# Performance work log

Hardware: AMD Instinct MI355X
Metric: run time of the kernel (lower is better)

Reference implementation:

```python
import jax, jax.numpy as jnp
import numpy as np

EPS = 1e-5
S_CENTERS = 1024  # npoint//4
NSAMPLE = 32


def index_points(pts, idx):
    # pts [B,N,C], idx [B,...] int -> [B,...,C]
    return jax.vmap(lambda p, i: p[i])(pts, idx)


def farthest_point_sample(xyz, npoint):
    # xyz [B,N,3] -> [B,npoint] indices (deterministic start at index 0)
    B, N, _ = xyz.shape
    def body(carry, _):
        dist, far = carry
        centroid = jnp.take_along_axis(xyz, far[:, None, None], axis=1)  # [B,1,3]
        d = jnp.sum((xyz - centroid) ** 2, axis=-1)                      # [B,N]
        dist = jnp.minimum(dist, d)
        nxt = jnp.argmax(dist, axis=-1).astype(jnp.int32)
        return (dist, nxt), far
    init = (jnp.full((B, N), 1e10, xyz.dtype), jnp.zeros((B,), jnp.int32))
    _, idx = jax.lax.scan(body, init, None, length=npoint)
    return jnp.transpose(idx)  # [B,npoint]


def knn_point(k, xyz, new_xyz):
    # squared dists [B,S,N], take k nearest
    d = (jnp.sum(new_xyz ** 2, -1)[:, :, None]
         + jnp.sum(xyz ** 2, -1)[:, None, :]
         - 2.0 * jnp.einsum('bsc,bnc->bsn', new_xyz, xyz))
    _, idx = jax.lax.top_k(-d, k)
    return idx  # [B,S,k]


def instance_norm(h):
    # h [B,S,K,C]: InstanceNorm2d (affine=False) normalizes per (b,c) over spatial dims
    mu = jnp.mean(h, axis=(1, 2), keepdims=True)
    var = jnp.var(h, axis=(1, 2), keepdims=True)
    return (h - mu) * jax.lax.rsqrt(var + EPS)


def setup_inputs() -> dict:
    key = jax.random.key(0)
    ks = jax.random.split(key, 12)
    B, N, C = 8, 4096, 128
    inp = {
        'pc1_l_loc2': jax.random.normal(ks[0], (B, 3, N), jnp.float32),
        'corr_feats': jax.random.normal(ks[1], (B, C, N), jnp.float32),
        'W1': jax.random.normal(ks[2], (128, 131), jnp.float32) * 0.05,
        'b1': jnp.zeros((128,), jnp.float32),
        'W2': jax.random.normal(ks[3], (128, 128), jnp.float32) * 0.05,
        'b2': jnp.zeros((128,), jnp.float32),
        'W3': jax.random.normal(ks[4], (128, 128), jnp.float32) * 0.05,
        'b3': jnp.zeros((128,), jnp.float32),
        'fc_w': jax.random.normal(ks[5], (3, 128), jnp.float32) * 0.05,
        'fc_b': jnp.zeros((3,), jnp.float32),
    }
    return inp


def reference(pc1_l_loc2, corr_feats, W1, b1, W2, b2, W3, b3, fc_w, fc_b):
    xyz = jnp.transpose(pc1_l_loc2, (0, 2, 1))    # [B,N,3]
    points = jnp.transpose(corr_feats, (0, 2, 1))  # [B,N,128]

    fps_idx = farthest_point_sample(xyz, S_CENTERS)           # [B,S]
    new_xyz = index_points(xyz, fps_idx)                      # [B,S,3]
    idx = knn_point(NSAMPLE, xyz, new_xyz)                    # [B,S,K]
    grouped_xyz = index_points(xyz, idx)                      # [B,S,K,3]
    grouped_xyz_norm = grouped_xyz - new_xyz[:, :, None, :]
    grouped_pts = index_points(points, idx)                   # [B,S,K,128]
    h = jnp.concatenate([grouped_xyz_norm, grouped_pts], -1)  # [B,S,K,131]

    for W, b in ((W1, b1), (W2, b2), (W3, b3)):
        h = jnp.einsum('bskc,oc->bsko', h, W) + b  # 1x1 conv as matmul
        h = jax.nn.relu(instance_norm(h))

    x = jnp.max(h, axis=2)                         # [B,S,128] max over neighbors
    x = jnp.einsum('bsc,oc->bso', x, fc_w) + fc_b  # [B,S,3]
    flow0 = jnp.transpose(x, (0, 2, 1))            # [B,3,S]
    return flow0
```

## Files before the change

### kernel.cpp

```cpp
#include <hip/hip_runtime.h>
#include <hip/hip_fp16.h>

#define NB 8
#define NPTS 4096
#define NS 1024
#define NK 32
#define NM (NB*NS*NK)

typedef _Float16 f16x8 __attribute__((ext_vector_type(8)));
typedef float    f32x4 __attribute__((ext_vector_type(4)));
typedef float    f32x2 __attribute__((ext_vector_type(2)));

__device__ __forceinline__ float bf2f(unsigned short u){ return __uint_as_float(((unsigned)u)<<16); }
__device__ __forceinline__ unsigned short f2bf(float f){
  unsigned u = __float_as_uint(f);
  u = u + 0x7fffu + ((u>>16)&1u);
  return (unsigned short)(u>>16);
}
__device__ __forceinline__ unsigned long long umax64(unsigned long long a, unsigned long long b){ return a>b?a:b; }

#define DPP_STEP_MAX(x, ctrl, rm) { \
  unsigned _t = (unsigned)__builtin_amdgcn_update_dpp((int)(x), (int)(x), (ctrl), (rm), 0xf, false); \
  (x) = ((x) > _t) ? (x) : _t; }

__device__ __forceinline__ unsigned wave_max_u32(unsigned x){
  DPP_STEP_MAX(x, 0x111, 0xf);
  DPP_STEP_MAX(x, 0x112, 0xf);
  DPP_STEP_MAX(x, 0x114, 0xf);
  DPP_STEP_MAX(x, 0x118, 0xf);
  DPP_STEP_MAX(x, 0x142, 0xa);
  DPP_STEP_MAX(x, 0x143, 0xc);
  return (unsigned)__builtin_amdgcn_readlane((int)x, 63);
}

__device__ __forceinline__ bool detect_f32(const unsigned short* __restrict__ u){
  int huge_=0, zero_=0;
  #pragma unroll
  for (int i=0;i<64;i++){
    unsigned short w = u[i];
    if ((w & 0x7fffu) == 0) { zero_++; continue; }
    float a = fabsf(bf2f(w));
    if (a > 1e6f || a < 1e-6f) huge_++;
  }
  return (huge_ >= 8) || (zero_ >= 24);
}
__device__ __forceinline__ float ldin(const void* p, size_t i, bool f32){
  if (f32) return ((const float*)p)[i];
  else     return bf2f(((const unsigned short*)p)[i]);
}

__global__ __launch_bounds__(256) void fps_kernel(const void* __restrict__ pc1,
                                                  int* __restrict__ fps_out){
  __shared__ __align__(16) float4 cp4[NPTS];
  __shared__ __align__(16) unsigned long long part[2][4];
  int b = blockIdx.x, t = threadIdx.x;
  const bool f32 = detect_f32((const unsigned short*)pc1);
  const size_t base = (size_t)b*3*NPTS;
  for (int i=t;i<NPTS;i+=256){
    float4 v;
    v.x = ldin(pc1, base+i, f32);
    v.y = ldin(pc1, base+NPTS+i, f32);
    v.z = ldin(pc1, base+2*NPTS+i, f32);
    v.w = 0.f;
    cp4[i] = v;
  }
  __syncthreads();
  f32x2 px[8],py[8],pz[8],dist[8];
  #pragma unroll
  for (int j=0;j<8;j++){
    float4 a = cp4[t*16+2*j], c = cp4[t*16+2*j+1];
    px[j] = f32x2{a.x, c.x};
    py[j] = f32x2{a.y, c.y};
    pz[j] = f32x2{a.z, c.z};
    dist[j] = f32x2{1e10f, 1e10f};
  }
  int far = 0;
  int w = t>>6, lane = t&63;
  for (int it=0; it<NS; it++){
    if (t==0) fps_out[b*NS+it] = far;
    float4 cc = cp4[far];
    f32x2 vcx = f32x2{cc.x,cc.x}, vcy = f32x2{cc.y,cc.y}, vcz = f32x2{cc.z,cc.z};
    {
      #pragma clang fp contract(off)
      #pragma unroll
      for (int j=0;j<8;j++){
        f32x2 dx = px[j]-vcx, dy = py[j]-vcy, dz = pz[j]-vcz;
        f32x2 d  = (dx*dx + dy*dy) + dz*dz;
        dist[j]  = __builtin_elementwise_min(dist[j], d);
      }
    }
    float d_[16];
    #pragma unroll
    for (int j=0;j<8;j++){ d_[2*j]=dist[j][0]; d_[2*j+1]=dist[j][1]; }
    float a0 = fmaxf(fmaxf(d_[0],d_[1]),d_[2]);
    float a1 = fmaxf(fmaxf(d_[3],d_[4]),d_[5]);
    float a2 = fmaxf(fmaxf(d_[6],d_[7]),d_[8]);
    float a3 = fmaxf(fmaxf(d_[9],d_[10]),d_[11]);
    float a4 = fmaxf(fmaxf(d_[12],d_[13]),d_[14]);
    float b0 = fmaxf(fmaxf(a0,a1),a2);
    float b1 = fmaxf(fmaxf(a3,a4),d_[15]);
    float bl = fmaxf(b0,b1);
    int li = 0;
    #pragma unroll
    for (int i=15;i>=0;i--) if (d_[i]==bl) li = i;
    unsigned blu = __float_as_uint(bl);
    unsigned wm = wave_max_u32(blu);
    unsigned long long mk = __ballot(blu == wm);
    int l = __builtin_ctzll(mk);
    int idx = __builtin_amdgcn_readlane(t*16+li, l);
    if (lane==0) part[it&1][w] = ((unsigned long long)wm<<32) | (unsigned)(NPTS-1-idx);
    __syncthreads();
    const ulonglong2* pp = (const ulonglong2*)&part[it&1][0];
    ulonglong2 A = pp[0], B = pp[1];
    unsigned long long m = umax64(umax64(A.x,A.y), umax64(B.x,B.y));
    far = NPTS-1 - (int)(m & 0xffffffffu);
  }
}

__global__ __launch_bounds__(256) void knn_kernel(const void* __restrict__ pc1,
                                                  const int* __restrict__ fps_idx,
                                                  float* __restrict__ new_xyz,
                                                  int* __restrict__ knn_idx){
  __shared__ __align__(16) unsigned hist[4096];
  __shared__ __align__(16) unsigned long long cand[512];
  __shared__ unsigned part[256];
  __shared__ unsigned sup[16];
  __shared__ unsigned scal[2];
  int blk = blockIdx.x;
  int b = blk >> 10;
  int t = threadIdx.x;
  const bool f32 = detect_f32((const unsigned short*)pc1);
  const size_t base = (size_t)b*3*NPTS;
  int n0 = fps_idx[blk];
  float qx = ldin(pc1, base+n0, f32);
  float qy = ldin(pc1, base+NPTS+n0, f32);
  float qz = ldin(pc1, base+2*NPTS+n0, f32);
  if (t==0){
    new_xyz[(size_t)blk*3]=qx; new_xyz[(size_t)blk*3+1]=qy; new_xyz[(size_t)blk*3+2]=qz;
    scal[0]=0u;
  }
  #pragma unroll
  for (int j=0;j<16;j++) hist[j*256 + t] = 0u;
  float qn = __fadd_rn(__fadd_rn(__fmul_rn(qx,qx),__fmul_rn(qy,qy)),__fmul_rn(qz,qz));
  unsigned dv[16];
  #pragma unroll
  for (int k=0;k<16;k++){
    int n = t + 256*k;
    float x = ldin(pc1, base+n, f32);
    float y = ldin(pc1, base+NPTS+n, f32);
    float z = ldin(pc1, base+2*NPTS+n, f32);
    float pn = __fadd_rn(__fadd_rn(__fmul_rn(x,x),__fmul_rn(y,y)),__fmul_rn(z,z));
    float dt = __fadd_rn(__fadd_rn(__fmul_rn(qx,x),__fmul_rn(qy,y)),__fmul_rn(qz,z));
    float d  = __fsub_rn(__fadd_rn(qn,pn), __fmul_rn(2.f,dt));
    unsigned u = __float_as_uint(d);
    dv[k] = (u & 0x80000000u) ? ~u : (u | 0x80000000u);
  }
  __syncthreads();
  #pragma unroll
  for (int k=0;k<16;k++)
    atomicAdd(&hist[dv[k]>>20], 1u);
  __syncthreads();
  {
    unsigned s = 0;
    const uint4* hp = (const uint4*)&hist[t*16];
    #pragma unroll
    for (int j=0;j<4;j++){
      uint4 v = hp[j];
      s += v.x + v.y + v.z + v.w;
    }
    part[t] = s;
  }
  __syncthreads();
  if (t < 16){
    unsigned q = 0;
    #pragma unroll
    for (int j=0;j<16;j++) q += part[t*16 + j];
    sup[t] = q;
  }
  __syncthreads();
  if (t == 0){
    unsigned acc = 0; int sb = 0;
    for (; sb < 16; sb++){ unsigned v = sup[sb]; if (acc + v >= NK) break; acc += v; }
    int pt = sb*16;
    for (; pt < sb*16+16; pt++){ unsigned v = part[pt]; if (acc + v >= NK) break; acc += v; }
    int bn = pt*16;
    for (; bn < pt*16+16; bn++){ unsigned v = hist[bn]; if (acc + v >= NK) break; acc += v; }
    scal[1] = (unsigned)bn;
  }
  __syncthreads();
  unsigned beta = scal[1];
  #pragma unroll
  for (int k=0;k<16;k++){
    if ((dv[k]>>20) <= beta){
      unsigned pos = atomicAdd(&scal[0], 1u);
      if (pos < 512u)
        cand[pos] = ((unsigned long long)dv[k]<<32) | (unsigned)(t + 256*k);
    }
  }
  __syncthreads();
  int C = (int)scal[0]; if (C > 512) C = 512;
  for (int tt = t; tt < C; tt += 256){
    unsigned long long K = cand[tt];
    int rank = 0;
    for (int j = 0; j < C; j++) rank += (cand[j] < K) ? 1 : 0;
    if (rank < NK) knn_idx[(size_t)blk*NK + rank] = (int)(K & 0xffffffffu);
  }
}

__global__ __launch_bounds__(256) void feat_transpose(const void* __restrict__ feats,
                                                      const void* __restrict__ pc1,
                                                      _Float16* __restrict__ G,
                                                      float* __restrict__ statz){
  __shared__ float tile[128][65];
  const bool f32 = detect_f32((const unsigned short*)pc1);
  int blk = blockIdx.x;
  int b = blk>>6, n0 = (blk&63)*64;
  int t = threadIdx.x;
  if (blk==0){
    for (int i=t;i<6144;i+=256) statz[i]=0.f;
  }
  #pragma unroll 4
  for (int i=0;i<32;i++){
    int idx = i*256 + t;
    int c = idx>>6, n = idx&63;
    tile[c][n] = ldin(feats, ((size_t)b*128 + c)*NPTS + n0 + n, f32);
  }
  __syncthreads();
  #pragma unroll 4
  for (int i=0;i<32;i++){
    int idx = i*256 + t;
    int n = idx>>7, c = idx&127;
    G[((size_t)b*NPTS + n0 + n)*136 + 3 + c] = (_Float16)tile[c][n];
  }
  if (t<64){
    size_t gb = ((size_t)b*NPTS + n0 + t)*136;
    G[gb]=(_Float16)0.f; G[gb+1]=(_Float16)0.f; G[gb+2]=(_Float16)0.f;
    #pragma unroll
    for (int c=131;c<136;c++) G[gb+c]=(_Float16)0.f;
  }
}

template<int LAYER>
__global__ __launch_bounds__(256) void conv_mfma(
    const void* __restrict__ pc1,
    const _Float16* __restrict__ G,
    const int* __restrict__ knn_idx,
    const float* __restrict__ new_xyz,
    const _Float16* __restrict__ Hin,
    const float* __restrict__ gp1,
    const float* __restrict__ gp2,
    const void* __restrict__ W,
    _Float16* __restrict__ Hout,
    float* __restrict__ gs1, float* __restrict__ gs2)
{
  constexpr int KC  = (LAYER==1)?131:128;
  constexpr int KCP = (LAYER==1)?160:128;
  constexpr int HSW = (LAYER==1)?168:136;
  __shared__ __align__(16) _Float16 hs[128][HSW];
  __shared__ __align__(16) _Float16 wt[128][40];
  __shared__ float red1[4][64], red2[4][64];
  __shared__ int   nidx[128];
  __shared__ float cxyz[4][3];
  __shared__ __align__(16) _Float16 smuh[128], srsh[128];
  int blk = blockIdx.x;
  int m0 = blk*128;
  int b  = m0 >> 15;
  int t  = threadIdx.x;
  const bool f32 = detect_f32((const unsigned short*)pc1);
  int w = t>>6, lane = t&63;
  int l16 = lane&15, q = lane>>4, q8 = q*8;
  int wr = (w&1)*64, wc = (w>>1)*64;

  if (LAYER==1){
    if (t<128) nidx[t] = knn_idx[m0+t];
    if (t<12)  cxyz[t/3][t%3] = new_xyz[(size_t)(m0>>5)*3 + t];
    __syncthreads();
    for (int u=t; u<128*17; u+=256){
      int p = u/17, qq = u - p*17;
      const f16x8* src = (const f16x8*)(G + ((size_t)b*NPTS + nidx[p])*136 + qq*8);
      *(f16x8*)&hs[p][qq*8] = *src;
    }
    for (int u=t; u<128*3; u+=256){
      int p = u/3, qq = u - p*3;
      uint4 z; z.x=z.y=z.z=z.w=0u;
      *(uint4*)&hs[p][136+qq*8] = z;
    }
    __syncthreads();
    if (t<128){
      int n = nidx[t];
      float cx = cxyz[t>>5][0], cy = cxyz[t>>5][1], cz = cxyz[t>>5][2];
      hs[t][0] = (_Float16)(ldin(pc1, ((size_t)b*3+0)*NPTS+n, f32) - cx);
      hs[t][1] = (_Float16)(ldin(pc1, ((size_t)b*3+1)*NPTS+n, f32) - cy);
      hs[t][2] = (_Float16)(ldin(pc1, ((size_t)b*3+2)*NPTS+n, f32) - cz);
    }
    __syncthreads();
  } else {
    if (t<128){
      const float inv = 1.0f/32768.0f;
      float m = gp1[b*128+t]*inv;
      smuh[t] = (_Float16)m;
      srsh[t] = (_Float16)rsqrtf(gp2[b*128+t]*inv - m*m + 1e-5f);
    }
    __syncthreads();
    int p = t & 127, hi = t>>7;
    const _Float16* src = Hin + (size_t)(m0+p)*128 + hi*64;
    f16x8 zero8 = {};
    #pragma unroll
    for (int j=0;j<8;j++){
      f16x8 v   = *(const f16x8*)(src + j*8);
      f16x8 mu8 = *(const f16x8*)&smuh[hi*64 + j*8];
      f16x8 rs8 = *(const f16x8*)&srsh[hi*64 + j*8];
      f16x8 o = (v - mu8) * rs8;
      o = __builtin_elementwise_max(o, zero8);
      *(f16x8*)&hs[p][hi*64 + j*8] = o;
    }
    __syncthreads();
  }

  f32x4 acc[4][4];
  #pragma unroll
  for (int i=0;i<4;i++)
    #pragma unroll
    for (int c=0;c<4;c++){ acc[i][c][0]=0.f; acc[i][c][1]=0.f; acc[i][c][2]=0.f; acc[i][c][3]=0.f; }

  for (int k0=0; k0<KCP; k0+=32){
    {
      int o = t>>1, half = t&1;
      f16x8 w0, w1;
      if (f32 && LAYER!=1){
        const float4* Wf = (const float4*)((const float*)W + (size_t)o*KC + k0 + half*16);
        float4 v0 = Wf[0], v1 = Wf[1], v2 = Wf[2], v3 = Wf[3];
        w0[0]=(_Float16)v0.x; w0[1]=(_Float16)v0.y; w0[2]=(_Float16)v0.z; w0[3]=(_Float16)v0.w;
        w0[4]=(_Float16)v1.x; w0[5]=(_Float16)v1.y; w0[6]=(_Float16)v1.z; w0[7]=(_Float16)v1.w;
        w1[0]=(_Float16)v2.x; w1[1]=(_Float16)v2.y; w1[2]=(_Float16)v2.z; w1[3]=(_Float16)v2.w;
        w1[4]=(_Float16)v3.x; w1[5]=(_Float16)v3.y; w1[6]=(_Float16)v3.z; w1[7]=(_Float16)v3.w;
      } else {
        #pragma unroll
        for (int jj=0;jj<8;jj++){
          int c0 = k0 + half*16 + jj, c1 = c0 + 8;
          w0[jj] = (_Float16)((c0<KC) ? ldin(W, (size_t)o*KC + c0, f32) : 0.f);
          w1[jj] = (_Float16)((c1<KC) ? ldin(W, (size_t)o*KC + c1, f32) : 0.f);
        }
      }
      *(f16x8*)&wt[o][half*16]     = w0;
      *(f16x8*)&wt[o][half*16 + 8] = w1;
    }
    __syncthreads();
    f16x8 av[4], bv[4];
    #pragma unroll
    for (int i=0;i<4;i++) av[i] = *(const f16x8*)&hs[wr + i*16 + l16][k0 + q8];
    #pragma unroll
    for (int c=0;c<4;c++) bv[c] = *(const f16x8*)&wt[wc + c*16 + l16][q8];
    #pragma unroll
    for (int i=0;i<4;i++)
      #pragma unroll
      for (int c=0;c<4;c++)
        acc[i][c] = __builtin_amdgcn_mfma_f32_16x16x32_f16(av[i], bv[c], acc[i][c], 0,0,0);
    __syncthreads();
  }

  #pragma unroll
  for (int c=0;c<4;c++){
    int o = wc + c*16 + l16;
    float s1=0.f, s2=0.f;
    #pragma unroll
    for (int i=0;i<4;i++){
      int row = wr + i*16 + q*4;
      #pragma unroll
      for (int r=0;r<4;r++){
        float v = acc[i][c][r];
        hs[row + r][o] = (_Float16)v;
        s1 += v; s2 = fmaf(v,v,s2);
      }
    }
    s1 += __shfl_xor(s1, 16, 64); s1 += __shfl_xor(s1, 32, 64);
    s2 += __shfl_xor(s2, 16, 64); s2 += __shfl_xor(s2, 32, 64);
    if (q==0){ red1[w][c*16+l16] = s1; red2[w][c*16+l16] = s2; }
  }
  __syncthreads();
  _Float16* dst0 = Hout + (size_t)m0*128;
  #pragma unroll
  for (int j=0;j<8;j++){
    int fi = j*256 + t;
    int row = fi >> 4, col = (fi & 15)*8;
    *(f16x8*)(dst0 + (size_t)fi*8) = *(const f16x8*)&hs[row][col];
  }
  if (t<128){
    int lo = t & 63, g = (t>>6)*2;
    unsafeAtomicAdd(&gs1[b*128+t], red1[g][lo] + red1[g+1][lo]);
    unsafeAtomicAdd(&gs2[b*128+t], red2[g][lo] + red2[g+1][lo]);
  }
}

__global__ __launch_bounds__(128) void final_kernel(
    const void* __restrict__ pc1,
    const _Float16* __restrict__ H,
    const float* __restrict__ gp1, const float* __restrict__ gp2,
    const void* __restrict__ fc_w, const void* __restrict__ fc_b,
    void* __restrict__ outv)
{
  int blk = blockIdx.x;
  int b = blk>>10, s = blk & 1023;
  int o = threadIdx.x;
  const bool f32 = detect_f32((const unsigned short*)pc1);
  int bo = b*128 + o;
  const float inv = 1.0f/32768.0f;
  float mu_ = gp1[bo]*inv;
  float rs_ = rsqrtf(gp2[bo]*inv - mu_*mu_ + 1e-5f);
  const _Float16* hp = H + (size_t)blk*NK*128 + o;
  float m = -1e30f;
  #pragma unroll 4
  for(int k=0;k<NK;k++){
    float v = ((float)hp[(size_t)k*128] - mu_)*rs_;
    m = fmaxf(m, v);
  }
  m = fmaxf(m, 0.f);
  __shared__ float mv[128];
  mv[o] = m;
  __syncthreads();
  if (o<3){
    float acc = ldin(fc_b, o, f32);
    for(int c=0;c<128;c++) acc = fmaf(ldin(fc_w, (size_t)o*128+c, f32), mv[c], acc);
    size_t oi = ((size_t)b*3 + o)*NS + s;
    if (f32) ((float*)outv)[oi] = acc;
    else     ((unsigned short*)outv)[oi] = f2bf(acc);
  }
}

extern "C" void kernel_launch(void* const* d_in, const int* in_sizes, int n_in,
                              void* d_out, int out_size, void* d_ws, size_t ws_size,
                              hipStream_t stream){
  const void* pc1   = d_in[0];
  const void* feats = d_in[1];
  const void* W1    = d_in[2];
  const void* W2    = d_in[4];
  const void* W3    = d_in[6];
  const void* fcw   = d_in[8];
  const void* fcb   = d_in[9];
  char* ws = (char*)d_ws;
  int*      fps  = (int*)     (ws + 0);
  float*    nxyz = (float*)   (ws + 32768);
  int*      knn  = (int*)     (ws + 131072);
  float*    st   = (float*)   (ws + 1179648);
  _Float16* Ha   = (_Float16*)(ws + 1204224);
  _Float16* Hb   = (_Float16*)(ws + 68313088);
  _Float16* G    = Hb;

  feat_transpose<<<NB*64, 256, 0, stream>>>(feats, pc1, G, st);
  fps_kernel<<<NB, 256, 0, stream>>>(pc1, fps);
  knn_kernel<<<NB*NS, 256, 0, stream>>>(pc1, fps, nxyz, knn);

  conv_mfma<1><<<NM/128, 256, 0, stream>>>(pc1, G, knn, nxyz,
      (const _Float16*)nullptr, (const float*)nullptr, (const float*)nullptr,
      W1, Ha, st, st+1024);
  conv_mfma<2><<<NM/128, 256, 0, stream>>>(pc1, G, knn, nxyz,
      Ha, st, st+1024, W2, Hb, st+2048, st+3072);
  conv_mfma<3><<<NM/128, 256, 0, stream>>>(pc1, G, knn, nxyz,
      Hb, st+2048, st+3072, W3, Ha, st+4096, st+5120);

  final_kernel<<<NB*NS, 128, 0, stream>>>(pc1, Ha, st+4096, st+5120, fcw, fcb, d_out);
}
```

Baseline: 1.059 ms.

## Fuse FPS with feature transpose; load conv weights directly into registers

Merges the FPS kernel and the feature-transpose kernel into one launch. The 8 FPS blocks then run alongside the transpose blocks instead of after them. For layers 2 and 3, the conv kernel now reads weight fragments straight from global memory into MFMA operands, dropping the LDS weight staging and the per-k-step barriers. It also adds a waves-per-EU hint. The final kernel stages each H tile into LDS with vectorized loads before the max reduction. Risks are the larger shared-memory footprint for the fused transpose blocks and redundant global weight reads in every block.

```diff
diff --git a/kernel.cpp b/kernel.cpp
--- a/kernel.cpp
+++ b/kernel.cpp
@@ -49,71 +49,104 @@
   else     return bf2f(((const unsigned short*)p)[i]);
 }
 
-__global__ __launch_bounds__(256) void fps_kernel(const void* __restrict__ pc1,
-                                                  int* __restrict__ fps_out){
-  __shared__ __align__(16) float4 cp4[NPTS];
-  __shared__ __align__(16) unsigned long long part[2][4];
-  int b = blockIdx.x, t = threadIdx.x;
+__global__ __launch_bounds__(256) void fps_fused(const void* __restrict__ pc1,
+                                                 const void* __restrict__ feats,
+                                                 int* __restrict__ fps_out,
+                                                 _Float16* __restrict__ G,
+                                                 float* __restrict__ statz){
+  __shared__ __align__(16) char smem[65600];
+  int t = threadIdx.x;
   const bool f32 = detect_f32((const unsigned short*)pc1);
-  const size_t base = (size_t)b*3*NPTS;
-  for (int i=t;i<NPTS;i+=256){
-    float4 v;
-    v.x = ldin(pc1, base+i, f32);
-    v.y = ldin(pc1, base+NPTS+i, f32);
-    v.z = ldin(pc1, base+2*NPTS+i, f32);
-    v.w = 0.f;
-    cp4[i] = v;
-  }
-  __syncthreads();
-  f32x2 px[8],py[8],pz[8],dist[8];
-  #pragma unroll
-  for (int j=0;j<8;j++){
-    float4 a = cp4[t*16+2*j], c = cp4[t*16+2*j+1];
-    px[j] = f32x2{a.x, c.x};
-    py[j] = f32x2{a.y, c.y};
-    pz[j] = f32x2{a.z, c.z};
-    dist[j] = f32x2{1e10f, 1e10f};
-  }
-  int far = 0;
-  int w = t>>6, lane = t&63;
-  for (int it=0; it<NS; it++){
-    if (t==0) fps_out[b*NS+it] = far;
-    float4 cc = cp4[far];
-    f32x2 vcx = f32x2{cc.x,cc.x}, vcy = f32x2{cc.y,cc.y}, vcz = f32x2{cc.z,cc.z};
-    {
-      #pragma clang fp contract(off)
-      #pragma unroll
-      for (int j=0;j<8;j++){
-        f32x2 dx = px[j]-vcx, dy = py[j]-vcy, dz = pz[j]-vcz;
-        f32x2 d  = (dx*dx + dy*dy) + dz*dz;
-        dist[j]  = __builtin_elementwise_min(dist[j], d);
+  if (blockIdx.x < 8){
+    float4* cp4 = (float4*)smem;
+    unsigned long long (*part)[4] = (unsigned long long (*)[4])(smem + 65536);
+    int b = blockIdx.x;
+    const size_t base = (size_t)b*3*NPTS;
+    for (int i=t;i<NPTS;i+=256){
+      float4 v;
+      v.x = ldin(pc1, base+i, f32);
+      v.y = ldin(pc1, base+NPTS+i, f32);
+      v.z = ldin(pc1, base+2*NPTS+i, f32);
+      v.w = 0.f;
+      cp4[i] = v;
+    }
+    __syncthreads();
+    f32x2 px[8],py[8],pz[8],dist[8];
+    #pragma unroll
+    for (int j=0;j<8;j++){
+      float4 a = cp4[t*16+2*j], c = cp4[t*16+2*j+1];
+      px[j] = f32x2{a.x, c.x};
+      py[j] = f32x2{a.y, c.y};
+      pz[j] = f32x2{a.z, c.z};
+      dist[j] = f32x2{1e10f, 1e10f};
+    }
+    int far = 0;
+    int w = t>>6, lane = t&63;
+    for (int it=0; it<NS; it++){
+      if (t==0) fps_out[b*NS+it] = far;
+      float4 cc = cp4[far];
+      f32x2 vcx = f32x2{cc.x,cc.x}, vcy = f32x2{cc.y,cc.y}, vcz = f32x2{cc.z,cc.z};
+      {
+        #pragma clang fp contract(off)
+        #pragma unroll
+        for (int j=0;j<8;j++){
+          f32x2 dx = px[j]-vcx, dy = py[j]-vcy, dz = pz[j]-vcz;
+          f32x2 d  = (dx*dx + dy*dy) + dz*dz;
+          dist[j]  = __builtin_elementwise_min(dist[j], d);
+        }
       }
-    }
-    float d_[16];
-    #pragma unroll
-    for (int j=0;j<8;j++){ d_[2*j]=dist[j][0]; d_[2*j+1]=dist[j][1]; }
-    float a0 = fmaxf(fmaxf(d_[0],d_[1]),d_[2]);
-    float a1 = fmaxf(fmaxf(d_[3],d_[4]),d_[5]);
-    float a2 = fmaxf(fmaxf(d_[6],d_[7]),d_[8]);
-    float a3 = fmaxf(fmaxf(d_[9],d_[10]),d_[11]);
-    float a4 = fmaxf(fmaxf(d_[12],d_[13]),d_[14]);
-    float b0 = fmaxf(fmaxf(a0,a1),a2);
-    float b1 = fmaxf(fmaxf(a3,a4),d_[15]);
-    float bl = fmaxf(b0,b1);
-    int li = 0;
-    #pragma unroll
-    for (int i=15;i>=0;i--) if (d_[i]==bl) li = i;
-    unsigned blu = __float_as_uint(bl);
-    unsigned wm = wave_max_u32(blu);
-    unsigned long long mk = __ballot(blu == wm);
-    int l = __builtin_ctzll(mk);
-    int idx = __builtin_amdgcn_readlane(t*16+li, l);
-    if (lane==0) part[it&1][w] = ((unsigned long long)wm<<32) | (unsigned)(NPTS-1-idx);
-    __syncthreads();
-    const ulonglong2* pp = (const ulonglong2*)&part[it&1][0];
-    ulonglong2 A = pp[0], B = pp[1];
-    unsigned long long m = umax64(umax64(A.x,A.y), umax64(B.x,B.y));
-    far = NPTS-1 - (int)(m & 0xffffffffu);
+      float d_[16];
+      #pragma unroll
+      for (int j=0;j<8;j++){ d_[2*j]=dist[j][0]; d_[2*j+1]=dist[j][1]; }
+      float a0 = fmaxf(fmaxf(d_[0],d_[1]),d_[2]);
+      float a1 = fmaxf(fmaxf(d_[3],d_[4]),d_[5]);
+      float a2 = fmaxf(fmaxf(d_[6],d_[7]),d_[8]);
+      float a3 = fmaxf(fmaxf(d_[9],d_[10]),d_[11]);
+      float a4 = fmaxf(fmaxf(d_[12],d_[13]),d_[14]);
+      float b0 = fmaxf(fmaxf(a0,a1),a2);
+      float b1 = fmaxf(fmaxf(a3,a4),d_[15]);
+      float bl = fmaxf(b0,b1);
+      int li = 0;
+      #pragma unroll
+      for (int i=15;i>=0;i--) if (d_[i]==bl) li = i;
+      unsigned blu = __float_as_uint(bl);
+      unsigned wm = wave_max_u32(blu);
+      unsigned long long mk = __ballot(blu == wm);
+      int l = __builtin_ctzll(mk);
+      int idx = __builtin_amdgcn_readlane(t*16+li, l);
+      if (lane==0) part[it&1][w] = ((unsigned long long)wm<<32) | (unsigned)(NPTS-1-idx);
+      __syncthreads();
+      const ulonglong2* pp = (const ulonglong2*)&part[it&1][0];
+      ulonglong2 A = pp[0], B = pp[1];
+      unsigned long long m = umax64(umax64(A.x,A.y), umax64(B.x,B.y));
+      far = NPTS-1 - (int)(m & 0xffffffffu);
+    }
+  } else {
+    float (*tile)[65] = (float (*)[65])smem;
+    int blk = blockIdx.x - 8;
+    int b = blk>>6, n0 = (blk&63)*64;
+    if (blk==0){
+      for (int i=t;i<6144;i+=256) statz[i]=0.f;
+    }
+    #pragma unroll 4
+    for (int i=0;i<32;i++){
+      int idx = i*256 + t;
+      int c = idx>>6, n = idx&63;
+      tile[c][n] = ldin(feats, ((size_t)b*128 + c)*NPTS + n0 + n, f32);
+    }
+    __syncthreads();
+    #pragma unroll 4
+    for (int i=0;i<32;i++){
+      int idx = i*256 + t;
+      int n = idx>>7, c = idx&127;
+      G[((size_t)b*NPTS + n0 + n)*136 + 3 + c] = (_Float16)tile[c][n];
+    }
+    if (t<64){
+      size_t gb = ((size_t)b*NPTS + n0 + t)*136;
+      G[gb]=(_Float16)0.f; G[gb+1]=(_Float16)0.f; G[gb+2]=(_Float16)0.f;
+      #pragma unroll
+      for (int c=131;c<136;c++) G[gb+c]=(_Float16)0.f;
+    }
   }
 }
 
@@ -207,41 +240,10 @@
   }
 }
 
-__global__ __launch_bounds__(256) void feat_transpose(const void* __restrict__ feats,
-                                                      const void* __restrict__ pc1,
-                                                      _Float16* __restrict__ G,
-                                                      float* __restrict__ statz){
-  __shared__ float tile[128][65];
-  const bool f32 = detect_f32((const unsigned short*)pc1);
-  int blk = blockIdx.x;
-  int b = blk>>6, n0 = (blk&63)*64;
-  int t = threadIdx.x;
-  if (blk==0){
-    for (int i=t;i<6144;i+=256) statz[i]=0.f;
-  }
-  #pragma unroll 4
-  for (int i=0;i<32;i++){
-    int idx = i*256 + t;
-    int c = idx>>6, n = idx&63;
-    tile[c][n] = ldin(feats, ((size_t)b*128 + c)*NPTS + n0 + n, f32);
-  }
-  __syncthreads();
-  #pragma unroll 4
-  for (int i=0;i<32;i++){
-    int idx = i*256 + t;
-    int n = idx>>7, c = idx&127;
-    G[((size_t)b*NPTS + n0 + n)*136 + 3 + c] = (_Float16)tile[c][n];
-  }
-  if (t<64){
-    size_t gb = ((size_t)b*NPTS + n0 + t)*136;
-    G[gb]=(_Float16)0.f; G[gb+1]=(_Float16)0.f; G[gb+2]=(_Float16)0.f;
-    #pragma unroll
-    for (int c=131;c<136;c++) G[gb+c]=(_Float16)0.f;
-  }
-}
-
 template<int LAYER>
-__global__ __launch_bounds__(256) void conv_mfma(
+__global__ __launch_bounds__(256)
+__attribute__((amdgpu_waves_per_eu(1,3)))
+void conv_mfma(
     const void* __restrict__ pc1,
     const _Float16* __restrict__ G,
     const int* __restrict__ knn_idx,
@@ -257,7 +259,7 @@
   constexpr int KCP = (LAYER==1)?160:128;
   constexpr int HSW = (LAYER==1)?168:136;
   __shared__ __align__(16) _Float16 hs[128][HSW];
-  __shared__ __align__(16) _Float16 wt[128][40];
+  __shared__ __align__(16) _Float16 wt[(LAYER==1)?128:1][40];
   __shared__ float red1[4][64], red2[4][64];
   __shared__ int   nidx[128];
   __shared__ float cxyz[4][3];
@@ -323,39 +325,64 @@
     #pragma unroll
     for (int c=0;c<4;c++){ acc[i][c][0]=0.f; acc[i][c][1]=0.f; acc[i][c][2]=0.f; acc[i][c][3]=0.f; }
 
-  for (int k0=0; k0<KCP; k0+=32){
-    {
-      int o = t>>1, half = t&1;
-      f16x8 w0, w1;
-      if (f32 && LAYER!=1){
-        const float4* Wf = (const float4*)((const float*)W + (size_t)o*KC + k0 + half*16);
-        float4 v0 = Wf[0], v1 = Wf[1], v2 = Wf[2], v3 = Wf[3];
-        w0[0]=(_Float16)v0.x; w0[1]=(_Float16)v0.y; w0[2]=(_Float16)v0.z; w0[3]=(_Float16)v0.w;
-        w0[4]=(_Float16)v1.x; w0[5]=(_Float16)v1.y; w0[6]=(_Float16)v1.z; w0[7]=(_Float16)v1.w;
-        w1[0]=(_Float16)v2.x; w1[1]=(_Float16)v2.y; w1[2]=(_Float16)v2.z; w1[3]=(_Float16)v2.w;
-        w1[4]=(_Float16)v3.x; w1[5]=(_Float16)v3.y; w1[6]=(_Float16)v3.z; w1[7]=(_Float16)v3.w;
-      } else {
+  if (LAYER==1){
+    for (int k0=0; k0<KCP; k0+=32){
+      {
+        int o = t>>1, half = t&1;
+        f16x8 w0, w1;
         #pragma unroll
         for (int jj=0;jj<8;jj++){
           int c0 = k0 + half*16 + jj, c1 = c0 + 8;
           w0[jj] = (_Float16)((c0<KC) ? ldin(W, (size_t)o*KC + c0, f32) : 0.f);
           w1[jj] = (_Float16)((c1<KC) ? ldin(W, (size_t)o*KC + c1, f32) : 0.f);
         }
+        *(f16x8*)&wt[o][half*16]     = w0;
+        *(f16x8*)&wt[o][half*16 + 8] = w1;
       }
-      *(f16x8*)&wt[o][half*16]     = w0;
-      *(f16x8*)&wt[o][half*16 + 8] = w1;
-    }
-    __syncthreads();
-    f16x8 av[4], bv[4];
-    #pragma unroll
-    for (int i=0;i<4;i++) av[i] = *(const f16x8*)&hs[wr + i*16 + l16][k0 + q8];
-    #pragma unroll
-    for (int c=0;c<4;c++) bv[c] = *(const f16x8*)&wt[wc + c*16 + l16][q8];
-    #pragma unroll
-    for (int i=0;i<4;i++)
-      #pragma unroll
-      for (int c=0;c<4;c++)
-        acc[i][c] = __builtin_amdgcn_mfma_f32_16x16x32_f16(av[i], bv[c], acc[i][c], 0,0,0);
+      __syncthreads();
+      f16x8 av[4], bv[4];
+      #pragma unroll
+      for (int i=0;i<4;i++) av[i] = *(const f16x8*)&hs[wr + i*16 + l16][k0 + q8];
+      #pragma unroll
+      for (int c=0;c<4;c++) bv[c] = *(const f16x8*)&wt[wc + c*16 + l16][q8];
+      #pragma unroll
+      for (int i=0;i<4;i++)
+        #pragma unroll
+        for (int c=0;c<4;c++)
+          acc[i][c] = __builtin_amdgcn_mfma_f32_16x16x32_f16(av[i], bv[c], acc[i][c], 0,0,0);
+      __syncthreads();
+    }
+  } else {
+    #pragma unroll
+    for (int k0=0; k0<128; k0+=32){
+      f16x8 av[4], bv[4];
+      #pragma unroll
+      for (int i=0;i<4;i++) av[i] = *(const f16x8*)&hs[wr + i*16 + l16][k0 + q8];
+      #pragma unroll
+      for (int c=0;c<4;c++){
+        int row = wc + c*16 + l16;
+        if (f32){
+          const f32x4* Wr = (const f32x4*)((const float*)W + (size_t)row*128 + k0 + q8);
+          f32x4 v0 = Wr[0], v1 = Wr[1];
+          f16x8 bb;
+          bb[0]=(_Float16)v0[0]; bb[1]=(_Float16)v0[1]; bb[2]=(_Float16)v0[2]; bb[3]=(_Float16)v0[3];
+          bb[4]=(_Float16)v1[0]; bb[5]=(_Float16)v1[1]; bb[6]=(_Float16)v1[2]; bb[7]=(_Float16)v1[3];
+          bv[c] = bb;
+        } else {
+          const ushort4* Wr = (const ushort4*)((const unsigned short*)W + (size_t)row*128 + k0 + q8);
+          ushort4 u0 = Wr[0], u1 = Wr[1];
+          f16x8 bb;
+          bb[0]=(_Float16)bf2f(u0.x); bb[1]=(_Float16)bf2f(u0.y); bb[2]=(_Float16)bf2f(u0.z); bb[3]=(_Float16)bf2f(u0.w);
+          bb[4]=(_Float16)bf2f(u1.x); bb[5]=(_Float16)bf2f(u1.y); bb[6]=(_Float16)bf2f(u1.z); bb[7]=(_Float16)bf2f(u1.w);
+          bv[c] = bb;
+        }
+      }
+      #pragma unroll
+      for (int i=0;i<4;i++)
+        #pragma unroll
+        for (int c=0;c<4;c++)
+          acc[i][c] = __builtin_amdgcn_mfma_f32_16x16x32_f16(av[i], bv[c], acc[i][c], 0,0,0);
+    }
     __syncthreads();
   }
 
@@ -399,23 +426,31 @@
     const void* __restrict__ fc_w, const void* __restrict__ fc_b,
     void* __restrict__ outv)
 {
+  __shared__ __align__(16) _Float16 tile[32][136];
+  __shared__ float mv[128];
   int blk = blockIdx.x;
   int b = blk>>10, s = blk & 1023;
   int o = threadIdx.x;
   const bool f32 = detect_f32((const unsigned short*)pc1);
+  const _Float16* src = H + (size_t)blk*NK*128;
+  #pragma unroll
+  for (int j=0;j<4;j++){
+    int fi = j*128 + o;
+    int row = fi >> 4, col = (fi & 15)*8;
+    *(f16x8*)&tile[row][col] = *(const f16x8*)(src + (size_t)fi*8);
+  }
+  __syncthreads();
   int bo = b*128 + o;
   const float inv = 1.0f/32768.0f;
   float mu_ = gp1[bo]*inv;
   float rs_ = rsqrtf(gp2[bo]*inv - mu_*mu_ + 1e-5f);
-  const _Float16* hp = H + (size_t)blk*NK*128 + o;
   float m = -1e30f;
   #pragma unroll 4
-  for(int k=0;k<NK;k++){
-    float v = ((float)hp[(size_t)k*128] - mu_)*rs_;
+  for (int k=0;k<NK;k++){
+    float v = ((float)tile[k][o] - mu_)*rs_;
     m = fmaxf(m, v);
   }
   m = fmaxf(m, 0.f);
-  __shared__ float mv[128];
   mv[o] = m;
   __syncthreads();
   if (o<3){
@@ -446,8 +481,7 @@
   _Float16* Hb   = (_Float16*)(ws + 68313088);
   _Float16* G    = Hb;
 
-  feat_transpose<<<NB*64, 256, 0, stream>>>(feats, pc1, G, st);
-  fps_kernel<<<NB, 256, 0, stream>>>(pc1, fps);
+  fps_fused<<<8 + NB*64, 256, 0, stream>>>(pc1, feats, fps, G, st);
   knn_kernel<<<NB*NS, 256, 0, stream>>>(pc1, fps, nxyz, knn);
 
   conv_mfma<1><<<NM/128, 256, 0, stream>>>(pc1, G, knn, nxyz,
```

After: 1.052 ms. No clear change (-0.7%).
